# Kernel tuning notes

Measured on AMD Instinct MI355X. Metric: run time of the kernel, lower is better.

The kernel has to match this reference:

```python
import jax, jax.numpy as jnp
import numpy as np

N_NODES = 50000
N_EDGES = 800000
IN_DIM = 128
HIDDEN = 128
OUT_DIM = 128


def setup_inputs() -> dict:
    key = jax.random.key(0)
    k1, k2, k3, k4, k5, k6 = jax.random.split(key, 6)
    X = jax.random.normal(k1, (N_NODES, IN_DIM), dtype=jnp.float32)
    W0 = jax.random.normal(k2, (HIDDEN, IN_DIM), dtype=jnp.float32) * (1.0 / np.sqrt(IN_DIM))
    W1 = jax.random.normal(k3, (OUT_DIM, HIDDEN), dtype=jnp.float32) * (1.0 / np.sqrt(HIDDEN))
    norm = jax.random.uniform(k4, (N_EDGES,), dtype=jnp.float32)
    src = jax.random.randint(k5, (N_EDGES,), 0, N_NODES, dtype=jnp.int32)
    dst = jax.random.randint(k6, (N_EDGES,), 0, N_NODES, dtype=jnp.int32)
    return {"X": X, "W0": W0, "W1": W1, "norm": norm, "src": src, "dst": dst}


def _propagate(S, src, dst, norm, n_nodes):
    # gather-scale-scatter: Z[dst] += S[src] * norm   (SpMM-style)
    msg = S[src] * norm[:, None]  # [E, d]
    return jax.ops.segment_sum(msg, dst, num_segments=n_nodes)


def reference(X, W0, W1, norm, src, dst):
    n = X.shape[0]
    # layer 1: linear (nn.Linear stores W as [out,in], so x @ W.T) + propagate + relu
    S0 = X @ W0.T                       # [N, hidden]
    H = jax.nn.relu(_propagate(S0, src, dst, norm, n))
    # dropout p=0.5 -> identity in eval mode (reference baseline)
    S1 = H @ W1.T                       # [N, out]
    Z = _propagate(S1, src, dst, norm, n)
    return (Z, H)
```

## Files before the change

### kernel.cpp

```cpp
#include <hip/hip_runtime.h>

#define DIM 128
#define NB 782
#define BCAP 1536
#define SC_VPT 16

typedef __attribute__((ext_vector_type(8))) short bf16x8_t;
typedef __attribute__((ext_vector_type(4))) float f32x4_t;

__device__ __forceinline__ short f2bf(float f) {
    unsigned u = __float_as_uint(f);
    u += 0x7FFFu + ((u >> 16) & 1u);
    return (short)(u >> 16);
}
__device__ __forceinline__ float bf2f(short s) {
    return __uint_as_float(((unsigned)(unsigned short)s) << 16);
}

__device__ __forceinline__ void gemm_body(const float* __restrict__ A,
                                          const float* __restrict__ W,
                                          short* __restrict__ Cbf, int n, int blk) {
    int wave = threadIdx.x >> 6;
    int lane = threadIdx.x & 63;
    int l16  = lane & 15;
    int quad = lane >> 4;
    int r0 = blk * 64 + wave * 16;

    int arow = r0 + l16;
    if (arow >= n) arow = n - 1;
    const float* Ar = A + (size_t)arow * DIM + quad * 8;

    bf16x8_t fa[4];
    #pragma unroll
    for (int kk = 0; kk < 4; kk++) {
        float4 x0 = *(const float4*)(Ar + kk * 32);
        float4 x1 = *(const float4*)(Ar + kk * 32 + 4);
        bf16x8_t f;
        f[0] = f2bf(x0.x); f[1] = f2bf(x0.y); f[2] = f2bf(x0.z); f[3] = f2bf(x0.w);
        f[4] = f2bf(x1.x); f[5] = f2bf(x1.y); f[6] = f2bf(x1.z); f[7] = f2bf(x1.w);
        fa[kk] = f;
    }

    #pragma unroll
    for (int ct = 0; ct < 8; ct++) {
        const float* Wr = W + (size_t)(ct * 16 + l16) * DIM + quad * 8;
        f32x4_t acc = {0.f, 0.f, 0.f, 0.f};
        #pragma unroll
        for (int kk = 0; kk < 4; kk++) {
            float4 w0 = *(const float4*)(Wr + kk * 32);
            float4 w1 = *(const float4*)(Wr + kk * 32 + 4);
            bf16x8_t fb;
            fb[0] = f2bf(w0.x); fb[1] = f2bf(w0.y); fb[2] = f2bf(w0.z); fb[3] = f2bf(w0.w);
            fb[4] = f2bf(w1.x); fb[5] = f2bf(w1.y); fb[6] = f2bf(w1.z); fb[7] = f2bf(w1.w);
            acc = __builtin_amdgcn_mfma_f32_16x16x32_bf16(fa[kk], fb, acc, 0, 0, 0);
        }
        #pragma unroll
        for (int j = 0; j < 4; j++) {
            int row = r0 + quad * 4 + j;
            if (row < n) Cbf[(size_t)row * DIM + ct * 16 + l16] = f2bf(acc[j]);
        }
    }
}

__device__ __forceinline__ void scatter_body(const int* __restrict__ src,
                                             const int* __restrict__ dst,
                                             const float* __restrict__ norm,
                                             int* __restrict__ bcursor,
                                             int2* __restrict__ binned, int E, int blk) {
    __shared__ int hist[NB];
    __shared__ int base[NB];
    int t = threadIdx.x;
    for (int b = t; b < NB; b += 256) hist[b] = 0;
    __syncthreads();

    int e0 = blk * (256 * SC_VPT);
    int bkts[SC_VPT];
    int pack[SC_VPT];
    int nrm[SC_VPT];
    #pragma unroll
    for (int k = 0; k < SC_VPT; k++) {
        int e = e0 + k * 256 + t;
        if (e < E) {
            int d = dst[e];
            bkts[k] = d >> 6;
            pack[k] = ((d & 63) << 26) | src[e];
            nrm[k]  = __float_as_int(norm[e]);
            atomicAdd(&hist[bkts[k]], 1);
        } else bkts[k] = -1;
    }
    __syncthreads();
    for (int b = t; b < NB; b += 256) {
        int c = hist[b];
        base[b] = b * BCAP + (c ? atomicAdd(&bcursor[b], c) : 0);
        hist[b] = 0;
    }
    __syncthreads();
    #pragma unroll
    for (int k = 0; k < SC_VPT; k++) {
        if (bkts[k] >= 0) {
            int pos = base[bkts[k]] + atomicAdd(&hist[bkts[k]], 1);
            binned[pos] = make_int2(pack[k], nrm[k]);
        }
    }
}

__global__ __launch_bounds__(256) void fused_gemm_scatter(
        const float* __restrict__ X, const float* __restrict__ W0,
        short* __restrict__ Sbf, int n,
        const int* __restrict__ src, const int* __restrict__ dst,
        const float* __restrict__ norm, int* __restrict__ bcursor,
        int2* __restrict__ binned, int E, int gemmBlocks) {
    if ((int)blockIdx.x < gemmBlocks)
        gemm_body(X, W0, Sbf, n, blockIdx.x);
    else
        scatter_body(src, dst, norm, bcursor, binned, E, blockIdx.x - gemmBlocks);
}

__global__ __launch_bounds__(256) void gemm_mfma(const float* __restrict__ A,
                                                 const float* __restrict__ W,
                                                 short* __restrict__ Cbf, int n) {
    gemm_body(A, W, Cbf, n, blockIdx.x);
}


__global__ __launch_bounds__(512) void prop_bucket(const short* __restrict__ Sbf,
                                                   const int2* __restrict__ binned,
                                                   const int* __restrict__ bcnt,
                                                   int2* __restrict__ edges2,
                                                   int* __restrict__ offs_g,
                                                   float* __restrict__ out,
                                                   int n, int do_relu, int mode) {
    __shared__ int2 raw[BCAP];
    __shared__ int2 eds[BCAP];
    __shared__ int  hist[64];
    __shared__ int  offs_s[65];
    int b = blockIdx.x;
    int t = threadIdx.x;

    if (mode == 0) {
        int cnt = bcnt[b];
        if (cnt > BCAP) cnt = BCAP;
        if (t < 64) hist[t] = 0;
        __syncthreads();
        const int2* eb = binned + (size_t)b * BCAP;
        for (int i = t; i < cnt; i += 512) {
            int2 e = eb[i];
            raw[i] = e;
            atomicAdd(&hist[((unsigned)e.x) >> 26], 1);
        }
        __syncthreads();
        if (t < 64) {
            int v = hist[t];
            int s = v;
            #pragma unroll
            for (int o = 1; o < 64; o <<= 1) {
                int x = __shfl_up(s, o, 64);
                if (t >= o) s += x;
            }
            offs_s[t] = s - v;
            if (t == 63) offs_s[64] = s;
            hist[t] = s - v;
        }
        __syncthreads();
        for (int i = t; i < cnt; i += 512) {
            int2 e = raw[i];
            int pos = atomicAdd(&hist[((unsigned)e.x) >> 26], 1);
            eds[pos] = e;
        }
        __syncthreads();
        int2* e2 = edges2 + (size_t)b * BCAP;
        for (int i = t; i < cnt; i += 512) e2[i] = eds[i];
        if (t < 65) offs_g[b * 65 + t] = offs_s[t];
    } else {
        if (t < 65) offs_s[t] = offs_g[b * 65 + t];
        __syncthreads();
    }

    int wv   = t >> 6;
    int lane = t & 63;
    int q    = lane >> 4;
    int l16  = lane & 15;
    int node0 = b << 6;
    const int2* eg = edges2 + (size_t)b * BCAP;

    for (int nd = wv; nd < 64; nd += 8) {
        int beg = offs_s[nd];
        int end = offs_s[nd + 1];
        float acc[8] = {};
        int i = beg + q;
        if (mode == 0) {
            for (; i + 4 < end; i += 8) {
                int2 e0 = eds[i];
                int2 e1 = eds[i + 4];
                bf16x8_t v0 = *(const bf16x8_t*)(Sbf + (size_t)((unsigned)e0.x & 0x3FFFFFF) * DIM + l16 * 8);
                bf16x8_t v1 = *(const bf16x8_t*)(Sbf + (size_t)((unsigned)e1.x & 0x3FFFFFF) * DIM + l16 * 8);
                float n0 = __int_as_float(e0.y);
                float n1 = __int_as_float(e1.y);
                #pragma unroll
                for (int j = 0; j < 8; j++) acc[j] += n0 * bf2f(v0[j]);
                #pragma unroll
                for (int j = 0; j < 8; j++) acc[j] += n1 * bf2f(v1[j]);
            }
            for (; i < end; i += 4) {
                int2 e = eds[i];
                bf16x8_t v = *(const bf16x8_t*)(Sbf + (size_t)((unsigned)e.x & 0x3FFFFFF) * DIM + l16 * 8);
                float nv = __int_as_float(e.y);
                #pragma unroll
                for (int j = 0; j < 8; j++) acc[j] += nv * bf2f(v[j]);
            }
        } else {
            for (; i + 4 < end; i += 8) {
                int2 e0 = eg[i];
                int2 e1 = eg[i + 4];
                bf16x8_t v0 = *(const bf16x8_t*)(Sbf + (size_t)((unsigned)e0.x & 0x3FFFFFF) * DIM + l16 * 8);
                bf16x8_t v1 = *(const bf16x8_t*)(Sbf + (size_t)((unsigned)e1.x & 0x3FFFFFF) * DIM + l16 * 8);
                float n0 = __int_as_float(e0.y);
                float n1 = __int_as_float(e1.y);
                #pragma unroll
                for (int j = 0; j < 8; j++) acc[j] += n0 * bf2f(v0[j]);
                #pragma unroll
                for (int j = 0; j < 8; j++) acc[j] += n1 * bf2f(v1[j]);
            }
            for (; i < end; i += 4) {
                int2 e = eg[i];
                bf16x8_t v = *(const bf16x8_t*)(Sbf + (size_t)((unsigned)e.x & 0x3FFFFFF) * DIM + l16 * 8);
                float nv = __int_as_float(e.y);
                #pragma unroll
                for (int j = 0; j < 8; j++) acc[j] += nv * bf2f(v[j]);
            }
        }
        #pragma unroll
        for (int j = 0; j < 8; j++) {
            acc[j] += __shfl_xor(acc[j], 16, 64);
            acc[j] += __shfl_xor(acc[j], 32, 64);
        }
        int node = node0 + nd;
        if (q == 0 && node < n) {
            if (do_relu) {
                #pragma unroll
                for (int j = 0; j < 8; j++) acc[j] = fmaxf(acc[j], 0.f);
            }
            f32x4_t o0 = {acc[0], acc[1], acc[2], acc[3]};
            f32x4_t o1 = {acc[4], acc[5], acc[6], acc[7]};
            float* row = out + (size_t)node * DIM + l16 * 8;
            __builtin_nontemporal_store(o0, (f32x4_t*)row);
            __builtin_nontemporal_store(o1, (f32x4_t*)(row + 4));
        }
    }
}


extern "C" void kernel_launch(void* const* d_in, const int* in_sizes, int n_in,
                              void* d_out, int out_size, void* d_ws, size_t ws_size,
                              hipStream_t stream) {
    const float* X    = (const float*)d_in[0];
    const float* W0   = (const float*)d_in[1];
    const float* W1   = (const float*)d_in[2];
    const float* norm = (const float*)d_in[3];
    const int*   src  = (const int*)d_in[4];
    const int*   dst  = (const int*)d_in[5];

    const int N = in_sizes[0] / DIM;
    const int E = in_sizes[3];

    float* Z = (float*)d_out;
    float* H = (float*)d_out + (size_t)N * DIM;

    char* ws = (char*)d_ws;
    short* Sbf    = (short*)ws;
    size_t off    = (size_t)N * DIM * sizeof(short);
    int*   bcursor= (int*)(ws + off); off += (NB * 4 + 255) / 256 * 256;
    int*   offs_g = (int*)(ws + off); off += ((size_t)NB * 65 * 4 + 255) / 256 * 256;
    int2*  binned = (int2*)(ws + off); off += (size_t)NB * BCAP * 8;
    int2*  edges2 = (int2*)(ws + off); off += (size_t)NB * BCAP * 8;

    const int gemmBlocks = (N + 63) / 64;
    const int scBlocks   = (E + 256 * SC_VPT - 1) / (256 * SC_VPT);

    hipMemsetAsync(bcursor, 0, NB * sizeof(int), stream);
    fused_gemm_scatter<<<gemmBlocks + scBlocks, 256, 0, stream>>>(
        X, W0, Sbf, N, src, dst, norm, bcursor, binned, E, gemmBlocks);
    prop_bucket<<<NB, 512, 0, stream>>>(Sbf, binned, bcursor, edges2, offs_g, H, N, 1, 0);
    gemm_mfma<<<gemmBlocks, 256, 0, stream>>>(H, W1, Sbf, N);
    prop_bucket<<<NB, 512, 0, stream>>>(Sbf, binned, bcursor, edges2, offs_g, Z, N, 0, 1);
}
```

Baseline: 224.4 us.

## Fuse second GEMM into first propagation kernel and pre-convert weights to bf16

Pre-converts W0 and W1 to bf16 in a small prep kernel that also zeroes the bucket cursors, replacing the memset and the per-block weight conversion. The first propagate kernel now runs the H @ W1ᵀ MFMA GEMM for its own 64 nodes right after writing H, reading H back from cache. This removes one launch and a separate pass over H. A second Sbf buffer is added so the fused GEMM output does not overwrite features other blocks are still gathering. The raw LDS staging buffer is dropped, and the second propagate becomes a gather-only kernel that reloads the pre-sorted edges into LDS.

```diff
diff --git a/kernel.cpp b/kernel.cpp
--- a/kernel.cpp
+++ b/kernel.cpp
@@ -6,6 +6,7 @@
 #define SC_VPT 16
 
 typedef __attribute__((ext_vector_type(8))) short bf16x8_t;
+typedef __attribute__((ext_vector_type(4))) short bf16x4_t;
 typedef __attribute__((ext_vector_type(4))) float f32x4_t;
 
 __device__ __forceinline__ short f2bf(float f) {
@@ -17,8 +18,31 @@
     return __uint_as_float(((unsigned)(unsigned short)s) << 16);
 }
 
+__global__ __launch_bounds__(256) void prep(const float* __restrict__ W0,
+                                            const float* __restrict__ W1,
+                                            short* __restrict__ W0bf,
+                                            short* __restrict__ W1bf,
+                                            int* __restrict__ bcursor) {
+    int b = blockIdx.x, t = threadIdx.x;
+    if (b == 0) {
+        for (int i = t; i < NB; i += 256) bcursor[i] = 0;
+    } else {
+        int tid = (b - 1) * 256 + t;
+        for (int i = tid; i < DIM * DIM / 4; i += 2048) {
+            float4 v = ((const float4*)W0)[i];
+            bf16x4_t o;
+            o[0] = f2bf(v.x); o[1] = f2bf(v.y); o[2] = f2bf(v.z); o[3] = f2bf(v.w);
+            ((bf16x4_t*)W0bf)[i] = o;
+            float4 u = ((const float4*)W1)[i];
+            bf16x4_t p;
+            p[0] = f2bf(u.x); p[1] = f2bf(u.y); p[2] = f2bf(u.z); p[3] = f2bf(u.w);
+            ((bf16x4_t*)W1bf)[i] = p;
+        }
+    }
+}
+
 __device__ __forceinline__ void gemm_body(const float* __restrict__ A,
-                                          const float* __restrict__ W,
+                                          const short* __restrict__ Wbf,
                                           short* __restrict__ Cbf, int n, int blk) {
     int wave = threadIdx.x >> 6;
     int lane = threadIdx.x & 63;
@@ -43,15 +67,11 @@
 
     #pragma unroll
     for (int ct = 0; ct < 8; ct++) {
-        const float* Wr = W + (size_t)(ct * 16 + l16) * DIM + quad * 8;
+        const short* Wr = Wbf + (size_t)(ct * 16 + l16) * DIM + quad * 8;
         f32x4_t acc = {0.f, 0.f, 0.f, 0.f};
         #pragma unroll
         for (int kk = 0; kk < 4; kk++) {
-            float4 w0 = *(const float4*)(Wr + kk * 32);
-            float4 w1 = *(const float4*)(Wr + kk * 32 + 4);
-            bf16x8_t fb;
-            fb[0] = f2bf(w0.x); fb[1] = f2bf(w0.y); fb[2] = f2bf(w0.z); fb[3] = f2bf(w0.w);
-            fb[4] = f2bf(w1.x); fb[5] = f2bf(w1.y); fb[6] = f2bf(w1.z); fb[7] = f2bf(w1.w);
+            bf16x8_t fb = *(const bf16x8_t*)(Wr + kk * 32);
             acc = __builtin_amdgcn_mfma_f32_16x16x32_bf16(fa[kk], fb, acc, 0, 0, 0);
         }
         #pragma unroll
@@ -105,129 +125,88 @@
 }
 
 __global__ __launch_bounds__(256) void fused_gemm_scatter(
-        const float* __restrict__ X, const float* __restrict__ W0,
+        const float* __restrict__ X, const short* __restrict__ W0bf,
         short* __restrict__ Sbf, int n,
         const int* __restrict__ src, const int* __restrict__ dst,
         const float* __restrict__ norm, int* __restrict__ bcursor,
         int2* __restrict__ binned, int E, int gemmBlocks) {
     if ((int)blockIdx.x < gemmBlocks)
-        gemm_body(X, W0, Sbf, n, blockIdx.x);
+        gemm_body(X, W0bf, Sbf, n, blockIdx.x);
     else
         scatter_body(src, dst, norm, bcursor, binned, E, blockIdx.x - gemmBlocks);
 }
 
-__global__ __launch_bounds__(256) void gemm_mfma(const float* __restrict__ A,
-                                                 const float* __restrict__ W,
-                                                 short* __restrict__ Cbf, int n) {
-    gemm_body(A, W, Cbf, n, blockIdx.x);
-}
-
-
-__global__ __launch_bounds__(512) void prop_bucket(const short* __restrict__ Sbf,
-                                                   const int2* __restrict__ binned,
-                                                   const int* __restrict__ bcnt,
-                                                   int2* __restrict__ edges2,
-                                                   int* __restrict__ offs_g,
-                                                   float* __restrict__ out,
-                                                   int n, int do_relu, int mode) {
-    __shared__ int2 raw[BCAP];
+__global__ __launch_bounds__(512) void prop_sort_gemm(
+        const short* __restrict__ Sbf, const int2* __restrict__ binned,
+        const int* __restrict__ bcnt, int2* __restrict__ edges2,
+        int* __restrict__ offs_g, float* __restrict__ H,
+        const short* __restrict__ W1bf, short* __restrict__ Cbf, int n) {
     __shared__ int2 eds[BCAP];
     __shared__ int  hist[64];
     __shared__ int  offs_s[65];
     int b = blockIdx.x;
     int t = threadIdx.x;
 
-    if (mode == 0) {
-        int cnt = bcnt[b];
-        if (cnt > BCAP) cnt = BCAP;
-        if (t < 64) hist[t] = 0;
-        __syncthreads();
-        const int2* eb = binned + (size_t)b * BCAP;
-        for (int i = t; i < cnt; i += 512) {
-            int2 e = eb[i];
-            raw[i] = e;
-            atomicAdd(&hist[((unsigned)e.x) >> 26], 1);
-        }
-        __syncthreads();
-        if (t < 64) {
-            int v = hist[t];
-            int s = v;
-            #pragma unroll
-            for (int o = 1; o < 64; o <<= 1) {
-                int x = __shfl_up(s, o, 64);
-                if (t >= o) s += x;
-            }
-            offs_s[t] = s - v;
-            if (t == 63) offs_s[64] = s;
-            hist[t] = s - v;
-        }
-        __syncthreads();
-        for (int i = t; i < cnt; i += 512) {
-            int2 e = raw[i];
-            int pos = atomicAdd(&hist[((unsigned)e.x) >> 26], 1);
-            eds[pos] = e;
-        }
-        __syncthreads();
-        int2* e2 = edges2 + (size_t)b * BCAP;
-        for (int i = t; i < cnt; i += 512) e2[i] = eds[i];
-        if (t < 65) offs_g[b * 65 + t] = offs_s[t];
-    } else {
-        if (t < 65) offs_s[t] = offs_g[b * 65 + t];
-        __syncthreads();
-    }
+    int cnt = bcnt[b];
+    if (cnt > BCAP) cnt = BCAP;
+    if (t < 64) hist[t] = 0;
+    __syncthreads();
+    const int2* eb = binned + (size_t)b * BCAP;
+    for (int i = t; i < cnt; i += 512)
+        atomicAdd(&hist[((unsigned)eb[i].x) >> 26], 1);
+    __syncthreads();
+    if (t < 64) {
+        int v = hist[t];
+        int s = v;
+        #pragma unroll
+        for (int o = 1; o < 64; o <<= 1) {
+            int x = __shfl_up(s, o, 64);
+            if (t >= o) s += x;
+        }
+        offs_s[t] = s - v;
+        if (t == 63) offs_s[64] = s;
+        hist[t] = s - v;
+    }
+    __syncthreads();
+    for (int i = t; i < cnt; i += 512) {
+        int2 e = eb[i];
+        int pos = atomicAdd(&hist[((unsigned)e.x) >> 26], 1);
+        eds[pos] = e;
+    }
+    __syncthreads();
+    int2* e2 = edges2 + (size_t)b * BCAP;
+    for (int i = t; i < cnt; i += 512) e2[i] = eds[i];
+    if (t < 65) offs_g[b * 65 + t] = offs_s[t];
 
     int wv   = t >> 6;
     int lane = t & 63;
     int q    = lane >> 4;
     int l16  = lane & 15;
     int node0 = b << 6;
-    const int2* eg = edges2 + (size_t)b * BCAP;
 
     for (int nd = wv; nd < 64; nd += 8) {
         int beg = offs_s[nd];
         int end = offs_s[nd + 1];
         float acc[8] = {};
         int i = beg + q;
-        if (mode == 0) {
-            for (; i + 4 < end; i += 8) {
-                int2 e0 = eds[i];
-                int2 e1 = eds[i + 4];
-                bf16x8_t v0 = *(const bf16x8_t*)(Sbf + (size_t)((unsigned)e0.x & 0x3FFFFFF) * DIM + l16 * 8);
-                bf16x8_t v1 = *(const bf16x8_t*)(Sbf + (size_t)((unsigned)e1.x & 0x3FFFFFF) * DIM + l16 * 8);
-                float n0 = __int_as_float(e0.y);
-                float n1 = __int_as_float(e1.y);
-                #pragma unroll
-                for (int j = 0; j < 8; j++) acc[j] += n0 * bf2f(v0[j]);
-                #pragma unroll
-                for (int j = 0; j < 8; j++) acc[j] += n1 * bf2f(v1[j]);
-            }
-            for (; i < end; i += 4) {
-                int2 e = eds[i];
-                bf16x8_t v = *(const bf16x8_t*)(Sbf + (size_t)((unsigned)e.x & 0x3FFFFFF) * DIM + l16 * 8);
-                float nv = __int_as_float(e.y);
-                #pragma unroll
-                for (int j = 0; j < 8; j++) acc[j] += nv * bf2f(v[j]);
-            }
-        } else {
-            for (; i + 4 < end; i += 8) {
-                int2 e0 = eg[i];
-                int2 e1 = eg[i + 4];
-                bf16x8_t v0 = *(const bf16x8_t*)(Sbf + (size_t)((unsigned)e0.x & 0x3FFFFFF) * DIM + l16 * 8);
-                bf16x8_t v1 = *(const bf16x8_t*)(Sbf + (size_t)((unsigned)e1.x & 0x3FFFFFF) * DIM + l16 * 8);
-                float n0 = __int_as_float(e0.y);
-                float n1 = __int_as_float(e1.y);
-                #pragma unroll
-                for (int j = 0; j < 8; j++) acc[j] += n0 * bf2f(v0[j]);
-                #pragma unroll
-                for (int j = 0; j < 8; j++) acc[j] += n1 * bf2f(v1[j]);
-            }
-            for (; i < end; i += 4) {
-                int2 e = eg[i];
-                bf16x8_t v = *(const bf16x8_t*)(Sbf + (size_t)((unsigned)e.x & 0x3FFFFFF) * DIM + l16 * 8);
-                float nv = __int_as_float(e.y);
-                #pragma unroll
-                for (int j = 0; j < 8; j++) acc[j] += nv * bf2f(v[j]);
-            }
+        for (; i + 4 < end; i += 8) {
+            int2 e0 = eds[i];
+            int2 e1 = eds[i + 4];
+            bf16x8_t v0 = *(const bf16x8_t*)(Sbf + (size_t)((unsigned)e0.x & 0x3FFFFFF) * DIM + l16 * 8);
+            bf16x8_t v1 = *(const bf16x8_t*)(Sbf + (size_t)((unsigned)e1.x & 0x3FFFFFF) * DIM + l16 * 8);
+            float n0 = __int_as_float(e0.y);
+            float n1 = __int_as_float(e1.y);
+            #pragma unroll
+            for (int j = 0; j < 8; j++) acc[j] += n0 * bf2f(v0[j]);
+            #pragma unroll
+            for (int j = 0; j < 8; j++) acc[j] += n1 * bf2f(v1[j]);
+        }
+        for (; i < end; i += 4) {
+            int2 e = eds[i];
+            bf16x8_t v = *(const bf16x8_t*)(Sbf + (size_t)((unsigned)e.x & 0x3FFFFFF) * DIM + l16 * 8);
+            float nv = __int_as_float(e.y);
+            #pragma unroll
+            for (int j = 0; j < 8; j++) acc[j] += nv * bf2f(v[j]);
         }
         #pragma unroll
         for (int j = 0; j < 8; j++) {
@@ -236,10 +215,103 @@
         }
         int node = node0 + nd;
         if (q == 0 && node < n) {
-            if (do_relu) {
-                #pragma unroll
-                for (int j = 0; j < 8; j++) acc[j] = fmaxf(acc[j], 0.f);
-            }
+            #pragma unroll
+            for (int j = 0; j < 8; j++) acc[j] = fmaxf(acc[j], 0.f);
+            f32x4_t o0 = {acc[0], acc[1], acc[2], acc[3]};
+            f32x4_t o1 = {acc[4], acc[5], acc[6], acc[7]};
+            float* row = H + (size_t)node * DIM + l16 * 8;
+            *(f32x4_t*)row = o0;
+            *(f32x4_t*)(row + 4) = o1;
+        }
+    }
+    __syncthreads();
+
+    int r0 = node0 + (wv & 3) * 16;
+    int arow = r0 + l16;
+    if (arow >= n) arow = n - 1;
+    const float* Ar = H + (size_t)arow * DIM + q * 8;
+    bf16x8_t fa[4];
+    #pragma unroll
+    for (int kk = 0; kk < 4; kk++) {
+        float4 x0 = *(const float4*)(Ar + kk * 32);
+        float4 x1 = *(const float4*)(Ar + kk * 32 + 4);
+        bf16x8_t f;
+        f[0] = f2bf(x0.x); f[1] = f2bf(x0.y); f[2] = f2bf(x0.z); f[3] = f2bf(x0.w);
+        f[4] = f2bf(x1.x); f[5] = f2bf(x1.y); f[6] = f2bf(x1.z); f[7] = f2bf(x1.w);
+        fa[kk] = f;
+    }
+    int ct0 = (wv >> 2) * 4;
+    #pragma unroll
+    for (int c = 0; c < 4; c++) {
+        int ct = ct0 + c;
+        const short* Wr = W1bf + (size_t)(ct * 16 + l16) * DIM + q * 8;
+        f32x4_t acc2 = {0.f, 0.f, 0.f, 0.f};
+        #pragma unroll
+        for (int kk = 0; kk < 4; kk++) {
+            bf16x8_t fb = *(const bf16x8_t*)(Wr + kk * 32);
+            acc2 = __builtin_amdgcn_mfma_f32_16x16x32_bf16(fa[kk], fb, acc2, 0, 0, 0);
+        }
+        #pragma unroll
+        for (int j = 0; j < 4; j++) {
+            int row = r0 + q * 4 + j;
+            if (row < n) Cbf[(size_t)row * DIM + ct * 16 + l16] = f2bf(acc2[j]);
+        }
+    }
+}
+
+__global__ __launch_bounds__(512) void prop_gather(const short* __restrict__ Sbf,
+                                                   const int2* __restrict__ edges2,
+                                                   const int* __restrict__ offs_g,
+                                                   float* __restrict__ out, int n) {
+    __shared__ int2 eds[BCAP];
+    __shared__ int  offs_s[65];
+    int b = blockIdx.x;
+    int t = threadIdx.x;
+
+    if (t < 65) offs_s[t] = offs_g[b * 65 + t];
+    __syncthreads();
+    int cnt = offs_s[64];
+    const int2* e2 = edges2 + (size_t)b * BCAP;
+    for (int i = t; i < cnt; i += 512) eds[i] = e2[i];
+    __syncthreads();
+
+    int wv   = t >> 6;
+    int lane = t & 63;
+    int q    = lane >> 4;
+    int l16  = lane & 15;
+    int node0 = b << 6;
+
+    for (int nd = wv; nd < 64; nd += 8) {
+        int beg = offs_s[nd];
+        int end = offs_s[nd + 1];
+        float acc[8] = {};
+        int i = beg + q;
+        for (; i + 4 < end; i += 8) {
+            int2 e0 = eds[i];
+            int2 e1 = eds[i + 4];
+            bf16x8_t v0 = *(const bf16x8_t*)(Sbf + (size_t)((unsigned)e0.x & 0x3FFFFFF) * DIM + l16 * 8);
+            bf16x8_t v1 = *(const bf16x8_t*)(Sbf + (size_t)((unsigned)e1.x & 0x3FFFFFF) * DIM + l16 * 8);
+            float n0 = __int_as_float(e0.y);
+            float n1 = __int_as_float(e1.y);
+            #pragma unroll
+            for (int j = 0; j < 8; j++) acc[j] += n0 * bf2f(v0[j]);
+            #pragma unroll
+            for (int j = 0; j < 8; j++) acc[j] += n1 * bf2f(v1[j]);
+        }
+        for (; i < end; i += 4) {
+            int2 e = eds[i];
+            bf16x8_t v = *(const bf16x8_t*)(Sbf + (size_t)((unsigned)e.x & 0x3FFFFFF) * DIM + l16 * 8);
+            float nv = __int_as_float(e.y);
+            #pragma unroll
+            for (int j = 0; j < 8; j++) acc[j] += nv * bf2f(v[j]);
+        }
+        #pragma unroll
+        for (int j = 0; j < 8; j++) {
+            acc[j] += __shfl_xor(acc[j], 16, 64);
+            acc[j] += __shfl_xor(acc[j], 32, 64);
+        }
+        int node = node0 + nd;
+        if (q == 0 && node < n) {
             f32x4_t o0 = {acc[0], acc[1], acc[2], acc[3]};
             f32x4_t o1 = {acc[4], acc[5], acc[6], acc[7]};
             float* row = out + (size_t)node * DIM + l16 * 8;
@@ -267,8 +339,11 @@
     float* H = (float*)d_out + (size_t)N * DIM;
 
     char* ws = (char*)d_ws;
-    short* Sbf    = (short*)ws;
+    short* Sbf0   = (short*)ws;
     size_t off    = (size_t)N * DIM * sizeof(short);
+    short* Sbf1   = (short*)(ws + off); off += (size_t)N * DIM * sizeof(short);
+    short* W0bf   = (short*)(ws + off); off += (size_t)DIM * DIM * sizeof(short);
+    short* W1bf   = (short*)(ws + off); off += (size_t)DIM * DIM * sizeof(short);
     int*   bcursor= (int*)(ws + off); off += (NB * 4 + 255) / 256 * 256;
     int*   offs_g = (int*)(ws + off); off += ((size_t)NB * 65 * 4 + 255) / 256 * 256;
     int2*  binned = (int2*)(ws + off); off += (size_t)NB * BCAP * 8;
@@ -277,10 +352,10 @@
     const int gemmBlocks = (N + 63) / 64;
     const int scBlocks   = (E + 256 * SC_VPT - 1) / (256 * SC_VPT);
 
-    hipMemsetAsync(bcursor, 0, NB * sizeof(int), stream);
+    prep<<<9, 256, 0, stream>>>(W0, W1, W0bf, W1bf, bcursor);
     fused_gemm_scatter<<<gemmBlocks + scBlocks, 256, 0, stream>>>(
-        X, W0, Sbf, N, src, dst, norm, bcursor, binned, E, gemmBlocks);
-    prop_bucket<<<NB, 512, 0, stream>>>(Sbf, binned, bcursor, edges2, offs_g, H, N, 1, 0);
-    gemm_mfma<<<gemmBlocks, 256, 0, stream>>>(H, W1, Sbf, N);
-    prop_bucket<<<NB, 512, 0, stream>>>(Sbf, binned, bcursor, edges2, offs_g, Z, N, 0, 1);
-}
+        X, W0bf, Sbf0, N, src, dst, norm, bcursor, binned, E, gemmBlocks);
+    prop_sort_gemm<<<NB, 512, 0, stream>>>(Sbf0, binned, bcursor, edges2, offs_g,
+                                           H, W1bf, Sbf1, N);
+    prop_gather<<<NB, 512, 0, stream>>>(Sbf1, edges2, offs_g, Z, N);
+}
```

After: 194.1 us. -13.5%, faster.
